# Performance work log

Hardware: AMD Instinct MI355X
Metric: run time of the kernel (lower is better)

## Reference

```python
import jax, jax.numpy as jnp
import numpy as np

EPS = 1e-5

def _layernorm(x, g, b):
    mu = jnp.mean(x, axis=-1, keepdims=True)
    var = jnp.mean(jnp.square(x - mu), axis=-1, keepdims=True)
    return (x - mu) * jax.lax.rsqrt(var + EPS) * g + b

def _knn_gather(x, idx):
    # x: (B, M, C), idx: (B, N, K) -> (B, N, K, C)
    return jax.vmap(lambda m, i: m[i])(x, idx)

def setup_inputs() -> dict:
    key = jax.random.key(0)
    B, N, M, K, C = 1, 8192, 8192, 32, 256
    ks = jax.random.split(key, 24)
    w = lambda k, *s: (jax.random.normal(k, s, dtype=jnp.float32) * 0.02)
    inp = {
        "input_states": jax.random.normal(ks[0], (B, N, C), dtype=jnp.float32),
        "memory_states": jax.random.normal(ks[1], (B, M, C), dtype=jnp.float32),
        "indices": jax.random.randint(ks[2], (B, N, K), 0, M, dtype=jnp.int32),
        "input_coord": jax.random.normal(ks[3], (B, N, 3), dtype=jnp.float32),
        "memory_coord": jax.random.normal(ks[4], (B, M, 3), dtype=jnp.float32),
        "attention_mask": jnp.ones((B, N, K), dtype=jnp.float32),
        "Wq": w(ks[5], C, C), "bq": jnp.zeros((C,), jnp.float32),
        "Wk": w(ks[6], C, C), "bk": jnp.zeros((C,), jnp.float32),
        "Wv": w(ks[7], C, C), "bv": jnp.zeros((C,), jnp.float32),
        "Wo": w(ks[8], C, C), "bo": jnp.zeros((C,), jnp.float32),
        "ln1_g": jnp.ones((C,), jnp.float32), "ln1_b": jnp.zeros((C,), jnp.float32),
        "Wrpe": w(ks[9], C // 2, 3), "brpe": jnp.zeros((C // 2,), jnp.float32),
        "We": w(ks[10], 2 * C, C), "be": jnp.zeros((2 * C,), jnp.float32),
        "Ws": w(ks[11], C, 2 * C), "bs": jnp.zeros((C,), jnp.float32),
        "ln2_g": jnp.ones((C,), jnp.float32), "ln2_b": jnp.zeros((C,), jnp.float32),
    }
    return inp

def reference(input_states, memory_states, indices, input_coord, memory_coord,
              attention_mask, Wq, bq, Wk, bk, Wv, bv, Wo, bo, ln1_g, ln1_b,
              Wrpe, brpe, We, be, Ws, bs, ln2_g, ln2_b):
    B, N, C = input_states.shape
    H = 8
    Ch = C // H
    q = input_states @ Wq.T + bq                                   # (B,N,C)
    k = _knn_gather(memory_states @ Wk.T + bk, indices)            # (B,N,K,C)
    v = _knn_gather(memory_states @ Wv.T + bv, indices)            # (B,N,K,C)
    # rotary positional encoding on relative coordinates
    rel = _knn_gather(memory_coord, indices) - input_coord[:, :, None, :]  # (B,N,K,3)
    ang = rel @ Wrpe.T + brpe                                      # (B,N,K,C/2)
    cos, sin = jnp.cos(ang), jnp.sin(ang)
    k2 = k.reshape(*k.shape[:-1], C // 2, 2)
    x0, x1 = k2[..., 0], k2[..., 1]
    k = jnp.stack([x0 * cos - x1 * sin, x0 * sin + x1 * cos], axis=-1).reshape(k.shape)
    # multi-head attention over K gathered neighbors
    qh = q.reshape(B, N, H, Ch)
    kh = k.reshape(B, N, -1, H, Ch)
    vh = v.reshape(B, N, -1, H, Ch)
    scores = jnp.einsum('bnhc,bnkhc->bhnk', qh, kh) / np.sqrt(Ch).astype(np.float32)
    scores = scores - 1e6 * (1.0 - attention_mask[:, None, :, :])
    attn = jax.nn.softmax(scores, axis=-1)
    hidden = jnp.einsum('bhnk,bnkhc->bnhc', attn, vh).reshape(B, N, C)
    hidden = hidden @ Wo.T + bo
    out = _layernorm(hidden + input_states, ln1_g, ln1_b)
    ff = jax.nn.relu(out @ We.T + be) @ Ws.T + bs
    return _layernorm(out + ff, ln2_g, ln2_b)
```

## Files before the change

### kernel.cpp

```cpp
#include <hip/hip_runtime.h>
#include <hip/hip_bf16.h>
#include <stdint.h>

typedef __attribute__((ext_vector_type(8))) __bf16 bf16x8;
typedef __attribute__((ext_vector_type(8))) unsigned short u16x8;
typedef __attribute__((ext_vector_type(4))) float f32x4;

__device__ inline float bf2f(unsigned short u) {
  union { unsigned u; float f; } z; z.u = ((unsigned)u) << 16; return z.f;
}
__device__ inline unsigned short f2bf(float f) {
  union { float f; unsigned u; } z; z.f = f;
  unsigned r = z.u + 0x7fffu + ((z.u >> 16) & 1u);
  return (unsigned short)(r >> 16);
}
__device__ inline void gload_lds16(const void* g, void* l) {
  __builtin_amdgcn_global_load_lds((const __attribute__((address_space(1))) void*)g,
                                   (__attribute__((address_space(3))) void*)l, 16, 0, 0);
}

__global__ __launch_bounds__(256) void wcvt(
    const float* __restrict__ Wq, const float* __restrict__ Wk, const float* __restrict__ Wv,
    const float* __restrict__ Wo, const float* __restrict__ We, const float* __restrict__ Ws,
    const float* __restrict__ Wrpe, const float* __restrict__ brpe,
    unsigned short* __restrict__ wqb, unsigned short* __restrict__ wkvb,
    unsigned short* __restrict__ wob, unsigned short* __restrict__ web,
    unsigned short* __restrict__ wsb, float4* __restrict__ rpe4) {
  const int b = blockIdx.x, t = threadIdx.x;
  const float* src; unsigned short* dst; long off;
  if (b < 64)       { src = Wq; dst = wqb;           off = (long)b * 1024; }
  else if (b < 128) { src = Wk; dst = wkvb;          off = (long)(b - 64) * 1024; }
  else if (b < 192) { src = Wv; dst = wkvb + 65536;  off = (long)(b - 128) * 1024; }
  else if (b < 256) { src = Wo; dst = wob;           off = (long)(b - 192) * 1024; }
  else if (b < 384) { src = We; dst = web;           off = (long)(b - 256) * 1024; }
  else if (b < 512) { src = Ws; dst = wsb;           off = (long)(b - 384) * 1024; }
  else {
    if (t < 128) {
      float4 r;
      r.x = Wrpe[3 * t]; r.y = Wrpe[3 * t + 1]; r.z = Wrpe[3 * t + 2]; r.w = brpe[t];
      rpe4[t] = r;
    }
    return;
  }
  const float4 v = *(const float4*)(src + off + t * 4);
  ushort4 o;
  o.x = f2bf(v.x); o.y = f2bf(v.y); o.z = f2bf(v.z); o.w = f2bf(v.w);
  *(ushort4*)(dst + off + t * 4) = o;
}

__global__ __launch_bounds__(256, 2) void gemm_proj(
    const float* __restrict__ x, const float* __restrict__ mem,
    const unsigned short* __restrict__ wqb, const unsigned short* __restrict__ wkvb,
    const float* __restrict__ bq, const float* __restrict__ bk, const float* __restrict__ bv,
    unsigned short* __restrict__ qbuf, unsigned short* __restrict__ kbp,
    unsigned short* __restrict__ vbp) {
  __shared__ __attribute__((aligned(16))) char lds[4096 + 8192];
  const int tid = threadIdx.x, lane = tid & 63;
  const int wm = tid >> 7, wo = (tid >> 6) & 1;
  const long bm = blockIdx.x;
  const int by = blockIdx.y;

  const float* Ab; const unsigned short* Wb; const float* biasp; unsigned short* outp; int cb;
  if (by < 2)      { Ab = x;   Wb = wqb  + by * 128 * 256;       biasp = bq + by * 128;       outp = qbuf; cb = by * 128; }
  else if (by < 4) { Ab = mem; Wb = wkvb + (by - 2) * 128 * 256; biasp = bk + (by - 2) * 128; outp = kbp;  cb = (by - 2) * 128; }
  else             { Ab = mem; Wb = wkvb + (by - 2) * 128 * 256; biasp = bv + (by - 4) * 128; outp = vbp;  cb = (by - 4) * 128; }

  f32x4 acc[2][4] = {};
  for (int kt = 0; kt < 8; ++kt) {
#pragma unroll
    for (int c = 0; c < 2; ++c) {
      const int fb = c * 4096 + tid * 16;
      const int row = fb >> 7, colb = fb & 127;
      const float4 a4 = *(const float4*)((const char*)Ab + (bm * 64 + row) * 1024 + kt * 128 + colb);
      ushort4 o;
      o.x = f2bf(a4.x); o.y = f2bf(a4.y); o.z = f2bf(a4.z); o.w = f2bf(a4.w);
      *(ushort4*)(lds + row * 64 + (colb >> 1)) = o;
    }
#pragma unroll
    for (int c = 0; c < 2; ++c) {
      const int fb = c * 4096 + tid * 16;
      gload_lds16((const char*)Wb + (long)(fb >> 6) * 512 + kt * 64 + (fb & 63), lds + 4096 + fb);
    }
    __syncthreads();
    bf16x8 af[2], bfr[4];
    const int kb = (lane >> 4) * 16;
#pragma unroll
    for (int i = 0; i < 2; ++i)
      af[i] = *(const bf16x8*)(lds + (wm * 32 + i * 16 + (lane & 15)) * 64 + kb);
#pragma unroll
    for (int j = 0; j < 4; ++j)
      bfr[j] = *(const bf16x8*)(lds + 4096 + (wo * 64 + j * 16 + (lane & 15)) * 64 + kb);
#pragma unroll
    for (int i = 0; i < 2; ++i)
#pragma unroll
      for (int j = 0; j < 4; ++j)
        acc[i][j] = __builtin_amdgcn_mfma_f32_16x16x32_bf16(af[i], bfr[j], acc[i][j], 0, 0, 0);
    __syncthreads();
  }

#pragma unroll
  for (int i = 0; i < 2; ++i) {
#pragma unroll
    for (int j = 0; j < 4; ++j) {
      const int lc = wo * 64 + j * 16 + (lane & 15);
      const float bvv = biasp[lc];
#pragma unroll
      for (int r = 0; r < 4; ++r) {
        const long rowg = bm * 64 + wm * 32 + i * 16 + (lane >> 4) * 4 + r;
        outp[rowg * 256 + cb + lc] = f2bf(acc[i][j][r] + bvv);
      }
    }
  }
}

__global__ __launch_bounds__(256, 2) void gemm_relu(
    const unsigned short* __restrict__ A,
    const unsigned short* __restrict__ W,
    const float* __restrict__ bias,
    unsigned short* __restrict__ outb) {
  __shared__ __attribute__((aligned(16))) char lds[(64 + 128) * 64];
  const int tid = threadIdx.x, lane = tid & 63;
  const int wm = tid >> 7, wo = (tid >> 6) & 1;
  const long bm = blockIdx.x, bo = blockIdx.y;

  f32x4 acc[2][4] = {};
  const char* Ab = (const char*)(A + bm * 64 * 256);
  const char* Wb = (const char*)(W + bo * 128 * 256);
  for (int kt = 0; kt < 8; ++kt) {
    {
      const int fb = tid * 16;
      gload_lds16(Ab + (long)(fb >> 6) * 512 + kt * 64 + (fb & 63), lds + fb);
    }
#pragma unroll
    for (int c = 0; c < 2; ++c) {
      const int fb = c * 4096 + tid * 16;
      gload_lds16(Wb + (long)(fb >> 6) * 512 + kt * 64 + (fb & 63), lds + 4096 + fb);
    }
    __syncthreads();
    bf16x8 af[2], bfr[4];
    const int kb = (lane >> 4) * 16;
#pragma unroll
    for (int i = 0; i < 2; ++i)
      af[i] = *(const bf16x8*)(lds + (wm * 32 + i * 16 + (lane & 15)) * 64 + kb);
#pragma unroll
    for (int j = 0; j < 4; ++j)
      bfr[j] = *(const bf16x8*)(lds + 4096 + (wo * 64 + j * 16 + (lane & 15)) * 64 + kb);
#pragma unroll
    for (int i = 0; i < 2; ++i)
#pragma unroll
      for (int j = 0; j < 4; ++j)
        acc[i][j] = __builtin_amdgcn_mfma_f32_16x16x32_bf16(af[i], bfr[j], acc[i][j], 0, 0, 0);
    __syncthreads();
  }
#pragma unroll
  for (int i = 0; i < 2; ++i) {
#pragma unroll
    for (int j = 0; j < 4; ++j) {
      const int colg = (int)bo * 128 + wo * 64 + j * 16 + (lane & 15);
      const float bvv = bias[colg];
#pragma unroll
      for (int r = 0; r < 4; ++r) {
        const long rowg = bm * 64 + wm * 32 + i * 16 + (lane >> 4) * 4 + r;
        const float v = acc[i][j][r] + bvv;
        outb[rowg * 512 + colg] = f2bf(v > 0.f ? v : 0.f);
      }
    }
  }
}

template <int KT, int WRITE_B>
__global__ __launch_bounds__(256, 2) void gemm_ln(
    const unsigned short* __restrict__ A,
    const unsigned short* __restrict__ W,
    const float* __restrict__ bias,
    const float* __restrict__ res,
    const float* __restrict__ g, const float* __restrict__ b,
    float* __restrict__ outf,
    unsigned short* __restrict__ outb) {
  __shared__ __attribute__((aligned(16))) char lds[2048 + 16384];
  __shared__ float2 part[2][32];
  const int tid = threadIdx.x, lane = tid & 63;
  const int wm = tid >> 7, wo = (tid >> 6) & 1;
  const long bm = blockIdx.x;
  constexpr int K = KT * 32;

  f32x4 acc[8] = {};
  const char* Ab = (const char*)(A + bm * 32 * (long)K);
  for (int kt = 0; kt < KT; ++kt) {
    if (tid < 128) {
      const int fb = tid * 16;
      gload_lds16(Ab + (long)(fb >> 6) * (K * 2) + kt * 64 + (fb & 63), lds + fb);
    }
#pragma unroll
    for (int c = 0; c < 4; ++c) {
      const int fb = c * 4096 + tid * 16;
      gload_lds16((const char*)W + (long)(fb >> 6) * (K * 2) + kt * 64 + (fb & 63), lds + 2048 + fb);
    }
    __syncthreads();
    bf16x8 af, bfr[8];
    const int kb = (lane >> 4) * 16;
    af = *(const bf16x8*)(lds + (wm * 16 + (lane & 15)) * 64 + kb);
#pragma unroll
    for (int j = 0; j < 8; ++j)
      bfr[j] = *(const bf16x8*)(lds + 2048 + (wo * 128 + j * 16 + (lane & 15)) * 64 + kb);
#pragma unroll
    for (int j = 0; j < 8; ++j)
      acc[j] = __builtin_amdgcn_mfma_f32_16x16x32_bf16(af, bfr[j], acc[j], 0, 0, 0);
    __syncthreads();
  }

  float gj[8], bj[8], biasj[8];
  int colg[8];
#pragma unroll
  for (int j = 0; j < 8; ++j) {
    colg[j] = wo * 128 + j * 16 + (lane & 15);
    gj[j] = g[colg[j]]; bj[j] = b[colg[j]]; biasj[j] = bias[colg[j]];
  }
  float v[8][4];
#pragma unroll
  for (int r = 0; r < 4; ++r) {
    const int row_local = wm * 16 + (lane >> 4) * 4 + r;
    const long rowg = bm * 32 + row_local;
    float s = 0.f, s2 = 0.f;
#pragma unroll
    for (int j = 0; j < 8; ++j) {
      float vv = acc[j][r] + biasj[j] + res[rowg * 256 + colg[j]];
      v[j][r] = vv;
      s += vv; s2 = fmaf(vv, vv, s2);
    }
#pragma unroll
    for (int m = 8; m > 0; m >>= 1) { s += __shfl_xor(s, m, 64); s2 += __shfl_xor(s2, m, 64); }
    if ((lane & 15) == 0) part[wo][row_local] = make_float2(s, s2);
  }
  __syncthreads();
#pragma unroll
  for (int r = 0; r < 4; ++r) {
    const int row_local = wm * 16 + (lane >> 4) * 4 + r;
    const long rowg = bm * 32 + row_local;
    const float2 p0 = part[0][row_local], p1 = part[1][row_local];
    const float mu = (p0.x + p1.x) * (1.f / 256.f);
    const float var = (p0.y + p1.y) * (1.f / 256.f) - mu * mu;
    const float inv = rsqrtf(var + 1e-5f);
#pragma unroll
    for (int j = 0; j < 8; ++j) {
      const float y = (v[j][r] - mu) * inv * gj[j] + bj[j];
      outf[rowg * 256 + colg[j]] = y;
      if (WRITE_B) outb[rowg * 256 + colg[j]] = f2bf(y);
    }
  }
}

__global__ __launch_bounds__(256, 4) void attn2(
    const unsigned short* __restrict__ qb,
    const unsigned short* __restrict__ kbp,
    const unsigned short* __restrict__ vbp,
    const int* __restrict__ idx,
    const float* __restrict__ icoord,
    const float* __restrict__ mcoord,
    const float* __restrict__ mask,
    const float4* __restrict__ rpe4,
    unsigned short* __restrict__ hb)
{
  __shared__ int idx_s[32];
  __shared__ float4 relm_s[32];
  __shared__ float4 rpe_s[128];
  __shared__ float p_s[256];
  __shared__ __attribute__((aligned(16))) unsigned short vls[32][256];

  const int n = blockIdx.x, t = threadIdx.x;
  if (t < 128) rpe_s[t] = rpe4[t];
  if (t < 32) {
    const int m = idx[n * 32 + t];
    idx_s[t] = m;
    float4 rm;
    rm.x = mcoord[(long)m * 3 + 0] - icoord[(long)n * 3 + 0];
    rm.y = mcoord[(long)m * 3 + 1] - icoord[(long)n * 3 + 1];
    rm.z = mcoord[(long)m * 3 + 2] - icoord[(long)n * 3 + 2];
    rm.w = mask[n * 32 + t];
    relm_s[t] = rm;
  }
  __syncthreads();

#pragma unroll
  for (int i = 0; i < 4; ++i) {
    const int b = i * 4096 + t * 16;
    const int r = b >> 9, cb = b & 511;
    gload_lds16((const char*)vbp + (long)idx_s[r] * 512 + cb, (char*)vls + b);
  }

  const int h = t >> 5, k = t & 31;
  const float4 rm = relm_s[k];
  const long krow = idx_s[k];

  u16x8 kv8[4], qv8[4];
  {
    const u16x8* kp = (const u16x8*)(kbp + krow * 256 + h * 32);
    const u16x8* qp = (const u16x8*)(qb + (long)n * 256 + h * 32);
#pragma unroll
    for (int i = 0; i < 4; ++i) { kv8[i] = kp[i]; qv8[i] = qp[i]; }
  }

  float sc = 0.f;
#pragma unroll
  for (int j2 = 0; j2 < 16; ++j2) {
    const float4 wj = rpe_s[h * 16 + j2];
    const float ang = fmaf(wj.x, rm.x, fmaf(wj.y, rm.y, fmaf(wj.z, rm.z, wj.w)));
    float sn, cs;
    __sincosf(ang, &sn, &cs);
    const int wi = j2 >> 2, e0 = (j2 & 3) * 2;
    const float x0 = bf2f(kv8[wi][e0]), x1 = bf2f(kv8[wi][e0 + 1]);
    const float q0 = bf2f(qv8[wi][e0]), q1 = bf2f(qv8[wi][e0 + 1]);
    const float k0 = fmaf(x0, cs, -x1 * sn);
    const float k1 = fmaf(x0, sn, x1 * cs);
    sc = fmaf(q0, k0, sc);
    sc = fmaf(q1, k1, sc);
  }
  sc = sc * 0.17677669529663687f - 1e6f * (1.f - rm.w);

  float mx = sc;
#pragma unroll
  for (int m = 16; m > 0; m >>= 1) mx = fmaxf(mx, __shfl_xor(mx, m, 32));
  const float e = __expf(sc - mx);
  float sum = e;
#pragma unroll
  for (int m = 16; m > 0; m >>= 1) sum += __shfl_xor(sum, m, 32);
  p_s[t] = e / sum;
  __syncthreads();

  float acc = 0.f;
  const int h2 = t >> 5;
#pragma unroll
  for (int k4 = 0; k4 < 8; ++k4) {
    const float4 p4 = *(const float4*)(p_s + h2 * 32 + k4 * 4);
    acc = fmaf(p4.x, bf2f(vls[k4 * 4 + 0][t]), acc);
    acc = fmaf(p4.y, bf2f(vls[k4 * 4 + 1][t]), acc);
    acc = fmaf(p4.z, bf2f(vls[k4 * 4 + 2][t]), acc);
    acc = fmaf(p4.w, bf2f(vls[k4 * 4 + 3][t]), acc);
  }
  hb[(long)n * 256 + t] = f2bf(acc);
}

extern "C" void kernel_launch(void* const* d_in, const int* in_sizes, int n_in,
                              void* d_out, int out_size, void* d_ws, size_t ws_size,
                              hipStream_t stream) {
  const float* x    = (const float*)d_in[0];
  const float* mem  = (const float*)d_in[1];
  const int* idx    = (const int*)d_in[2];
  const float* ic   = (const float*)d_in[3];
  const float* mc   = (const float*)d_in[4];
  const float* mask = (const float*)d_in[5];
  const float* Wq = (const float*)d_in[6];  const float* bq = (const float*)d_in[7];
  const float* Wk = (const float*)d_in[8];  const float* bk = (const float*)d_in[9];
  const float* Wv = (const float*)d_in[10]; const float* bv = (const float*)d_in[11];
  const float* Wo = (const float*)d_in[12]; const float* bo = (const float*)d_in[13];
  const float* g1 = (const float*)d_in[14]; const float* b1 = (const float*)d_in[15];
  const float* Wrpe = (const float*)d_in[16]; const float* brpe = (const float*)d_in[17];
  const float* We = (const float*)d_in[18]; const float* be = (const float*)d_in[19];
  const float* Ws = (const float*)d_in[20]; const float* bs = (const float*)d_in[21];
  const float* g2 = (const float*)d_in[22]; const float* b2 = (const float*)d_in[23];

  char* w = (char*)d_ws;
  const size_t MB = 1ull << 20;
  unsigned short* kbp   = (unsigned short*)(w + 0);
  unsigned short* vbp   = (unsigned short*)(w + 4 * MB);
  unsigned short* qbuf  = (unsigned short*)(w + 8 * MB);
  unsigned short* hb    = (unsigned short*)(w + 12 * MB);
  float*          out1  = (float*)(w + 16 * MB);
  unsigned short* out1b = (unsigned short*)(w + 24 * MB);
  unsigned short* ffb   = (unsigned short*)(w + 28 * MB);
  unsigned short* wqb  = (unsigned short*)(w + 36 * MB);
  unsigned short* wkvb = wqb + 65536;
  unsigned short* wob  = wkvb + 131072;
  unsigned short* web  = wob + 65536;
  unsigned short* wsb  = web + 131072;
  float4*         rpe4 = (float4*)(wsb + 131072);

  wcvt<<<513, 256, 0, stream>>>(Wq, Wk, Wv, Wo, We, Ws, Wrpe, brpe,
                                wqb, wkvb, wob, web, wsb, rpe4);

  gemm_proj<<<dim3(128, 6), 256, 0, stream>>>(x, mem, wqb, wkvb, bq, bk, bv, qbuf, kbp, vbp);

  attn2<<<8192, 256, 0, stream>>>(qbuf, kbp, vbp, idx, ic, mc, mask, rpe4, hb);

  gemm_ln<8, 1><<<256, 256, 0, stream>>>(hb, wob, bo, x, g1, b1, out1, out1b);

  gemm_relu<<<dim3(128, 4), 256, 0, stream>>>(out1b, web, be, ffb);

  gemm_ln<16, 0><<<256, 256, 0, stream>>>(ffb, wsb, bs, out1, g2, b2, (float*)d_out, nullptr);
}
```

Measured before the change: 90.72 us.

## Fuse weight conversion into projection GEMM, halve LN-GEMM tiles, drop fp32 residual

Removes the separate weight-conversion kernel. The QKV projection now converts fp32 weights to bf16 inline, and an extra grid row converts the Wo/We/Ws/RPE weights used by later kernels. The LayerNorm GEMMs switch to 16-row tiles with four waves splitting the columns, which doubles the grid to 512 blocks. The first LN output is written only in bf16 and reused as the second residual, which saves a launch and fp32 traffic but lowers residual precision and adds per-tile conversion work in the projection.

```diff
diff --git a/kernel.cpp b/kernel.cpp
--- a/kernel.cpp
+++ b/kernel.cpp
@@ -19,51 +19,55 @@
                                    (__attribute__((address_space(3))) void*)l, 16, 0, 0);
 }
 
-__global__ __launch_bounds__(256) void wcvt(
+__global__ __launch_bounds__(256, 2) void gemm_proj(
+    const float* __restrict__ x, const float* __restrict__ mem,
     const float* __restrict__ Wq, const float* __restrict__ Wk, const float* __restrict__ Wv,
     const float* __restrict__ Wo, const float* __restrict__ We, const float* __restrict__ Ws,
     const float* __restrict__ Wrpe, const float* __restrict__ brpe,
-    unsigned short* __restrict__ wqb, unsigned short* __restrict__ wkvb,
+    const float* __restrict__ bq, const float* __restrict__ bk, const float* __restrict__ bv,
+    unsigned short* __restrict__ qbuf, unsigned short* __restrict__ kbp,
+    unsigned short* __restrict__ vbp,
     unsigned short* __restrict__ wob, unsigned short* __restrict__ web,
     unsigned short* __restrict__ wsb, float4* __restrict__ rpe4) {
-  const int b = blockIdx.x, t = threadIdx.x;
-  const float* src; unsigned short* dst; long off;
-  if (b < 64)       { src = Wq; dst = wqb;           off = (long)b * 1024; }
-  else if (b < 128) { src = Wk; dst = wkvb;          off = (long)(b - 64) * 1024; }
-  else if (b < 192) { src = Wv; dst = wkvb + 65536;  off = (long)(b - 128) * 1024; }
-  else if (b < 256) { src = Wo; dst = wob;           off = (long)(b - 192) * 1024; }
-  else if (b < 384) { src = We; dst = web;           off = (long)(b - 256) * 1024; }
-  else if (b < 512) { src = Ws; dst = wsb;           off = (long)(b - 384) * 1024; }
-  else {
-    if (t < 128) {
-      float4 r;
-      r.x = Wrpe[3 * t]; r.y = Wrpe[3 * t + 1]; r.z = Wrpe[3 * t + 2]; r.w = brpe[t];
-      rpe4[t] = r;
+  const int tid = threadIdx.x;
+  const int by = blockIdx.y;
+  const long bm = blockIdx.x;
+
+  if (by == 6) {
+#pragma unroll
+    for (int it = 0; it < 3; ++it) {
+      const int j = (int)bm + 128 * it;
+      if (j < 64) {
+        const float4 v = *(const float4*)(Wo + (long)j * 1024 + tid * 4);
+        ushort4 o; o.x = f2bf(v.x); o.y = f2bf(v.y); o.z = f2bf(v.z); o.w = f2bf(v.w);
+        *(ushort4*)(wob + (long)j * 1024 + tid * 4) = o;
+      } else if (j < 192) {
+        const float4 v = *(const float4*)(We + (long)(j - 64) * 1024 + tid * 4);
+        ushort4 o; o.x = f2bf(v.x); o.y = f2bf(v.y); o.z = f2bf(v.z); o.w = f2bf(v.w);
+        *(ushort4*)(web + (long)(j - 64) * 1024 + tid * 4) = o;
+      } else if (j < 320) {
+        const float4 v = *(const float4*)(Ws + (long)(j - 192) * 1024 + tid * 4);
+        ushort4 o; o.x = f2bf(v.x); o.y = f2bf(v.y); o.z = f2bf(v.z); o.w = f2bf(v.w);
+        *(ushort4*)(wsb + (long)(j - 192) * 1024 + tid * 4) = o;
+      } else if (j == 320) {
+        if (tid < 128) {
+          float4 r;
+          r.x = Wrpe[3 * tid]; r.y = Wrpe[3 * tid + 1]; r.z = Wrpe[3 * tid + 2]; r.w = brpe[tid];
+          rpe4[tid] = r;
+        }
+      }
     }
     return;
   }
-  const float4 v = *(const float4*)(src + off + t * 4);
-  ushort4 o;
-  o.x = f2bf(v.x); o.y = f2bf(v.y); o.z = f2bf(v.z); o.w = f2bf(v.w);
-  *(ushort4*)(dst + off + t * 4) = o;
-}
-
-__global__ __launch_bounds__(256, 2) void gemm_proj(
-    const float* __restrict__ x, const float* __restrict__ mem,
-    const unsigned short* __restrict__ wqb, const unsigned short* __restrict__ wkvb,
-    const float* __restrict__ bq, const float* __restrict__ bk, const float* __restrict__ bv,
-    unsigned short* __restrict__ qbuf, unsigned short* __restrict__ kbp,
-    unsigned short* __restrict__ vbp) {
+
   __shared__ __attribute__((aligned(16))) char lds[4096 + 8192];
-  const int tid = threadIdx.x, lane = tid & 63;
+  const int lane = tid & 63;
   const int wm = tid >> 7, wo = (tid >> 6) & 1;
-  const long bm = blockIdx.x;
-  const int by = blockIdx.y;
-
-  const float* Ab; const unsigned short* Wb; const float* biasp; unsigned short* outp; int cb;
-  if (by < 2)      { Ab = x;   Wb = wqb  + by * 128 * 256;       biasp = bq + by * 128;       outp = qbuf; cb = by * 128; }
-  else if (by < 4) { Ab = mem; Wb = wkvb + (by - 2) * 128 * 256; biasp = bk + (by - 2) * 128; outp = kbp;  cb = (by - 2) * 128; }
-  else             { Ab = mem; Wb = wkvb + (by - 2) * 128 * 256; biasp = bv + (by - 4) * 128; outp = vbp;  cb = (by - 4) * 128; }
+
+  const float* Ab; const float* Wf; const float* biasp; unsigned short* outp; int cb;
+  if (by < 2)      { Ab = x;   Wf = Wq + (long)by * 128 * 256;       biasp = bq + by * 128;       outp = qbuf; cb = by * 128; }
+  else if (by < 4) { Ab = mem; Wf = Wk + (long)(by - 2) * 128 * 256; biasp = bk + (by - 2) * 128; outp = kbp;  cb = (by - 2) * 128; }
+  else             { Ab = mem; Wf = Wv + (long)(by - 4) * 128 * 256; biasp = bv + (by - 4) * 128; outp = vbp;  cb = (by - 4) * 128; }
 
   f32x4 acc[2][4] = {};
   for (int kt = 0; kt < 8; ++kt) {
@@ -72,14 +76,16 @@
       const int fb = c * 4096 + tid * 16;
       const int row = fb >> 7, colb = fb & 127;
       const float4 a4 = *(const float4*)((const char*)Ab + (bm * 64 + row) * 1024 + kt * 128 + colb);
-      ushort4 o;
-      o.x = f2bf(a4.x); o.y = f2bf(a4.y); o.z = f2bf(a4.z); o.w = f2bf(a4.w);
+      ushort4 o; o.x = f2bf(a4.x); o.y = f2bf(a4.y); o.z = f2bf(a4.z); o.w = f2bf(a4.w);
       *(ushort4*)(lds + row * 64 + (colb >> 1)) = o;
     }
 #pragma unroll
-    for (int c = 0; c < 2; ++c) {
+    for (int c = 0; c < 4; ++c) {
       const int fb = c * 4096 + tid * 16;
-      gload_lds16((const char*)Wb + (long)(fb >> 6) * 512 + kt * 64 + (fb & 63), lds + 4096 + fb);
+      const int row = fb >> 7, colb = fb & 127;
+      const float4 a4 = *(const float4*)((const char*)Wf + (long)row * 1024 + kt * 128 + colb);
+      ushort4 o; o.x = f2bf(a4.x); o.y = f2bf(a4.y); o.z = f2bf(a4.z); o.w = f2bf(a4.w);
+      *(ushort4*)(lds + 4096 + row * 64 + (colb >> 1)) = o;
     }
     __syncthreads();
     bf16x8 af[2], bfr[4];
@@ -168,84 +174,88 @@
   }
 }
 
-template <int KT, int WRITE_B>
+template <int KT, int OUT_BF16, int RES_BF16>
 __global__ __launch_bounds__(256, 2) void gemm_ln(
     const unsigned short* __restrict__ A,
     const unsigned short* __restrict__ W,
     const float* __restrict__ bias,
-    const float* __restrict__ res,
+    const float* __restrict__ resf,
+    const unsigned short* __restrict__ resb,
     const float* __restrict__ g, const float* __restrict__ b,
     float* __restrict__ outf,
     unsigned short* __restrict__ outb) {
-  __shared__ __attribute__((aligned(16))) char lds[2048 + 16384];
-  __shared__ float2 part[2][32];
+  __shared__ __attribute__((aligned(16))) char lds[1024 + 16384];
+  __shared__ float2 part[4][16];
   const int tid = threadIdx.x, lane = tid & 63;
-  const int wm = tid >> 7, wo = (tid >> 6) & 1;
+  const int wo = tid >> 6;
   const long bm = blockIdx.x;
   constexpr int K = KT * 32;
 
-  f32x4 acc[8] = {};
-  const char* Ab = (const char*)(A + bm * 32 * (long)K);
+  f32x4 acc[4] = {};
+  const char* Ab = (const char*)(A + bm * 16 * (long)K);
   for (int kt = 0; kt < KT; ++kt) {
-    if (tid < 128) {
+    if (tid < 64) {
       const int fb = tid * 16;
       gload_lds16(Ab + (long)(fb >> 6) * (K * 2) + kt * 64 + (fb & 63), lds + fb);
     }
 #pragma unroll
     for (int c = 0; c < 4; ++c) {
       const int fb = c * 4096 + tid * 16;
-      gload_lds16((const char*)W + (long)(fb >> 6) * (K * 2) + kt * 64 + (fb & 63), lds + 2048 + fb);
-    }
-    __syncthreads();
-    bf16x8 af, bfr[8];
+      gload_lds16((const char*)W + (long)(fb >> 6) * (K * 2) + kt * 64 + (fb & 63), lds + 1024 + fb);
+    }
+    __syncthreads();
+    bf16x8 af, bfr[4];
     const int kb = (lane >> 4) * 16;
-    af = *(const bf16x8*)(lds + (wm * 16 + (lane & 15)) * 64 + kb);
-#pragma unroll
-    for (int j = 0; j < 8; ++j)
-      bfr[j] = *(const bf16x8*)(lds + 2048 + (wo * 128 + j * 16 + (lane & 15)) * 64 + kb);
-#pragma unroll
-    for (int j = 0; j < 8; ++j)
+    af = *(const bf16x8*)(lds + ((lane & 15)) * 64 + kb);
+#pragma unroll
+    for (int j = 0; j < 4; ++j)
+      bfr[j] = *(const bf16x8*)(lds + 1024 + (wo * 64 + j * 16 + (lane & 15)) * 64 + kb);
+#pragma unroll
+    for (int j = 0; j < 4; ++j)
       acc[j] = __builtin_amdgcn_mfma_f32_16x16x32_bf16(af, bfr[j], acc[j], 0, 0, 0);
     __syncthreads();
   }
 
-  float gj[8], bj[8], biasj[8];
-  int colg[8];
-#pragma unroll
-  for (int j = 0; j < 8; ++j) {
-    colg[j] = wo * 128 + j * 16 + (lane & 15);
+  float gj[4], bj[4], biasj[4];
+  int colg[4];
+#pragma unroll
+  for (int j = 0; j < 4; ++j) {
+    colg[j] = wo * 64 + j * 16 + (lane & 15);
     gj[j] = g[colg[j]]; bj[j] = b[colg[j]]; biasj[j] = bias[colg[j]];
   }
-  float v[8][4];
+  float v[4][4];
 #pragma unroll
   for (int r = 0; r < 4; ++r) {
-    const int row_local = wm * 16 + (lane >> 4) * 4 + r;
-    const long rowg = bm * 32 + row_local;
+    const int row_local = (lane >> 4) * 4 + r;
+    const long rowg = bm * 16 + row_local;
     float s = 0.f, s2 = 0.f;
 #pragma unroll
-    for (int j = 0; j < 8; ++j) {
-      float vv = acc[j][r] + biasj[j] + res[rowg * 256 + colg[j]];
+    for (int j = 0; j < 4; ++j) {
+      const float rv = RES_BF16 ? bf2f(resb[rowg * 256 + colg[j]]) : resf[rowg * 256 + colg[j]];
+      float vv = acc[j][r] + biasj[j] + rv;
       v[j][r] = vv;
       s += vv; s2 = fmaf(vv, vv, s2);
     }
 #pragma unroll
-    for (int m = 8; m > 0; m >>= 1) { s += __shfl_xor(s, m, 64); s2 += __shfl_xor(s2, m, 64); }
+    for (int m = 8; m > 0; m >>= 1) { s += __shfl_xor(s, m, 16); s2 += __shfl_xor(s2, m, 16); }
     if ((lane & 15) == 0) part[wo][row_local] = make_float2(s, s2);
   }
   __syncthreads();
 #pragma unroll
   for (int r = 0; r < 4; ++r) {
-    const int row_local = wm * 16 + (lane >> 4) * 4 + r;
-    const long rowg = bm * 32 + row_local;
-    const float2 p0 = part[0][row_local], p1 = part[1][row_local];
-    const float mu = (p0.x + p1.x) * (1.f / 256.f);
-    const float var = (p0.y + p1.y) * (1.f / 256.f) - mu * mu;
+    const int row_local = (lane >> 4) * 4 + r;
+    const long rowg = bm * 16 + row_local;
+    float s = 0.f, s2 = 0.f;
+#pragma unroll
+    for (int wq = 0; wq < 4; ++wq) { s += part[wq][row_local].x; s2 += part[wq][row_local].y; }
+    const float mu = s * (1.f / 256.f);
+    const float var = s2 * (1.f / 256.f) - mu * mu;
     const float inv = rsqrtf(var + 1e-5f);
 #pragma unroll
-    for (int j = 0; j < 8; ++j) {
+    for (int j = 0; j < 4; ++j) {
       const float y = (v[j][r] - mu) * inv * gj[j] + bj[j];
-      outf[rowg * 256 + colg[j]] = y;
-      if (WRITE_B) outb[rowg * 256 + colg[j]] = f2bf(y);
+      if (OUT_BF16) outb[rowg * 256 + colg[j]] = f2bf(y);
+      else outf[rowg * 256 + colg[j]] = y;
     }
   }
 }
@@ -328,10 +338,9 @@
   __syncthreads();
 
   float acc = 0.f;
-  const int h2 = t >> 5;
 #pragma unroll
   for (int k4 = 0; k4 < 8; ++k4) {
-    const float4 p4 = *(const float4*)(p_s + h2 * 32 + k4 * 4);
+    const float4 p4 = *(const float4*)(p_s + (t >> 5) * 32 + k4 * 4);
     acc = fmaf(p4.x, bf2f(vls[k4 * 4 + 0][t]), acc);
     acc = fmaf(p4.y, bf2f(vls[k4 * 4 + 1][t]), acc);
     acc = fmaf(p4.z, bf2f(vls[k4 * 4 + 2][t]), acc);
@@ -365,26 +374,24 @@
   unsigned short* vbp   = (unsigned short*)(w + 4 * MB);
   unsigned short* qbuf  = (unsigned short*)(w + 8 * MB);
   unsigned short* hb    = (unsigned short*)(w + 12 * MB);
-  float*          out1  = (float*)(w + 16 * MB);
-  unsigned short* out1b = (unsigned short*)(w + 24 * MB);
-  unsigned short* ffb   = (unsigned short*)(w + 28 * MB);
-  unsigned short* wqb  = (unsigned short*)(w + 36 * MB);
-  unsigned short* wkvb = wqb + 65536;
-  unsigned short* wob  = wkvb + 131072;
+  unsigned short* out1b = (unsigned short*)(w + 16 * MB);
+  unsigned short* ffb   = (unsigned short*)(w + 20 * MB);
+  unsigned short* wob  = (unsigned short*)(w + 28 * MB);
   unsigned short* web  = wob + 65536;
   unsigned short* wsb  = web + 131072;
   float4*         rpe4 = (float4*)(wsb + 131072);
 
-  wcvt<<<513, 256, 0, stream>>>(Wq, Wk, Wv, Wo, We, Ws, Wrpe, brpe,
-                                wqb, wkvb, wob, web, wsb, rpe4);
-
-  gemm_proj<<<dim3(128, 6), 256, 0, stream>>>(x, mem, wqb, wkvb, bq, bk, bv, qbuf, kbp, vbp);
+  gemm_proj<<<dim3(128, 7), 256, 0, stream>>>(
+      x, mem, Wq, Wk, Wv, Wo, We, Ws, Wrpe, brpe, bq, bk, bv,
+      qbuf, kbp, vbp, wob, web, wsb, rpe4);
 
   attn2<<<8192, 256, 0, stream>>>(qbuf, kbp, vbp, idx, ic, mc, mask, rpe4, hb);
 
-  gemm_ln<8, 1><<<256, 256, 0, stream>>>(hb, wob, bo, x, g1, b1, out1, out1b);
+  gemm_ln<8, 1, 0><<<512, 256, 0, stream>>>(
+      hb, wob, bo, x, nullptr, g1, b1, nullptr, out1b);
 
   gemm_relu<<<dim3(128, 4), 256, 0, stream>>>(out1b, web, be, ffb);
 
-  gemm_ln<16, 0><<<256, 256, 0, stream>>>(ffb, wsb, bs, out1, g2, b2, (float*)d_out, nullptr);
-}
+  gemm_ln<16, 0, 1><<<512, 256, 0, stream>>>(
+      ffb, wsb, bs, nullptr, out1b, g2, b2, (float*)d_out, nullptr);
+}
```

After: 82.64 us. 8.9% less time.
